# Performance work log

Hardware: AMD Instinct MI355X
Metric: run time of the kernel (lower is better)

Reference implementation:

```python
import jax, jax.numpy as jnp
import numpy as np

MIN_LEN = 4      # g.min_word_length
MAX_LEN = 10     # g.max_word_length
THRESH = 0.05    # g.init_threshold
NEG = -1e9


def setup_inputs() -> dict:
    key = jax.random.key(0)
    ks = jax.random.split(key, 6)
    B, L, F, D, U, V = 16, 64, 60, 256, 600, 10000
    x = jax.random.normal(ks[0], (B, L, F), jnp.float32)            # batch dense feat matrix
    unit_feats = jax.random.normal(ks[1], (U, F), jnp.float32)      # per-unit features
    W = jax.random.normal(ks[2], (F, D), jnp.float32) * 0.1         # FeatEmbedding weight
    lengths = jax.random.randint(ks[3], (B,), MIN_LEN, L + 1)       # sentence lengths
    indexed_segments = jax.random.randint(ks[4], (V, MAX_LEN), 0, U)  # vocab -> unit ids
    vocab_length = jax.random.randint(ks[5], (V,), MIN_LEN, MAX_LEN + 1)
    return dict(x=x, unit_feats=unit_feats, W=W, lengths=lengths,
                indexed_segments=indexed_segments, vocab_length=vocab_length)


def reference(x, unit_feats, W, lengths, indexed_segments, vocab_length):
    B, L, _ = x.shape
    V, J = indexed_segments.shape
    # embedding: features -> char_emb space
    word_repr = x @ W                 # [B, L, D]
    unit_repr = unit_feats @ W        # [U, D]
    # cosine similarity between every segment position and every unit
    wn = word_repr / (jnp.linalg.norm(word_repr, axis=-1, keepdims=True) + 1e-8)
    un = unit_repr / (jnp.linalg.norm(unit_repr, axis=-1, keepdims=True) + 1e-8)
    sim = jnp.einsum('bld,ud->blu', wn, un)  # [B, L, U]
    # pad so span gathers past the end read zeros (masked later by `viable`)
    sim_pad = jnp.pad(sim, ((0, 0), (0, J), (0, 0)))
    # accumulate per-position unit scores along each vocab word's unit sequence
    acc = jnp.zeros((B, L, V), sim.dtype)
    per_len = []
    for j in range(J):  # fixed small loop over word-length positions
        # sim at start+j for unit indexed_segments[v, j] -> [B, L, V]
        s_j = sim_pad[:, j:j + L, :][:, :, indexed_segments[:, j]]
        acc = acc + s_j
        if j + 1 >= MIN_LEN:
            per_len.append(acc / (j + 1))  # length-normalized match score
    scores = jnp.stack(per_len, axis=2)  # [B, len_s=L, len_e=E, V]
    E = scores.shape[2]
    k = jnp.arange(E) + MIN_LEN                          # candidate word lengths
    ends = jnp.arange(L)[:, None] + k[None, :] - 1        # [L, E]
    viable = ends[None] < lengths[:, None, None]          # [B, L, E]
    len_match = vocab_length[None, None, None, :] == k[None, None, :, None]
    mask = viable[..., None] & len_match                  # [B, L, E, V]
    masked = jnp.where(mask, scores, NEG)
    # best vocab word per span candidate
    value = masked.max(axis=-1)                           # [B, L, E]
    matched_vocab = masked.argmax(axis=-1)                # [B, L, E]
    matched = value > THRESH
    # best span candidate per batch element (eval path: hard max)
    flat = value.reshape(B, -1)                           # [B, L*E]
    best_inds = flat.argmax(axis=-1)
    best_scores = flat.max(axis=-1)
    best_starts = best_inds // E
    best_ends = best_inds % E + best_starts + MIN_LEN - 1
    any_matched = matched.reshape(B, -1).any(axis=-1)
    best_vocab = jnp.take_along_axis(matched_vocab.reshape(B, -1), best_inds[:, None], axis=1)[:, 0]
    return best_scores, best_starts, best_ends, any_matched, best_vocab
```

## Files before the change

### kernel.cpp

```cpp
#include <hip/hip_runtime.h>
#include <math.h>

#define BB 16
#define LL 64
#define FF 60
#define DD 256
#define UU 600
#define VV 10000
#define JMAX 10
#define MINL 4
#define EE 7
#define NEG (-1e9f)
#define TH 0.05f
#define VHALF (VV / 2)

#define UNT_OFF   0
#define UNT_SZ    (256 * 640)
#define WNT_OFF   (UNT_OFF + UNT_SZ)
#define WNT_SZ    (256 * 1024)
#define SIM_OFF   (WNT_OFF + WNT_SZ)
#define SIM_SZ    (BB * LL * UU)
#define PK_OFF    (SIM_OFF + SIM_SZ)
#define PK_SZ     (VV * 8)
#define VAL_OFF   (PK_OFF + PK_SZ)
#define VAL_SZ    (2 * BB * LL * EE)
#define VOC_OFF   (VAL_OFF + VAL_SZ)

__global__ __launch_bounds__(256) void k_pack(const int* __restrict__ seg,
                                              const int* __restrict__ vlen,
                                              unsigned int* __restrict__ pk) {
    int v = blockIdx.x * 256 + threadIdx.x;
    if (v >= VV) return;
    const int* s = seg + v * JMAX;
    unsigned int t[10];
#pragma unroll
    for (int j = 0; j < JMAX; ++j) t[j] = (unsigned int)(s[j] * 11 + j);
    unsigned int* dst = pk + v * 8;
    dst[0] = t[0] | (t[1] << 16);
    dst[1] = t[2] | (t[3] << 16);
    dst[2] = t[4] | (t[5] << 16);
    dst[3] = t[6] | (t[7] << 16);
    dst[4] = t[8] | (t[9] << 16);
    dst[5] = (unsigned int)vlen[v];
    dst[6] = 0;
    dst[7] = 0;
}

__global__ __launch_bounds__(64) void k_embed(const float* __restrict__ x,
                                              const float* __restrict__ uf,
                                              const float* __restrict__ W,
                                              float* __restrict__ unT,
                                              float* __restrict__ wnT) {
    int id = blockIdx.x;
    int lane = threadIdx.x;
    const float* row;
    float* outB;
    int stride, col;
    if (id < UU) { row = uf + id * FF; outB = unT; stride = 640;  col = id; }
    else { int bl = id - UU; row = x + bl * FF; outB = wnT; stride = 1024; col = bl; }

    float r0 = 0.f, r1 = 0.f, r2 = 0.f, r3 = 0.f;
#pragma unroll 4
    for (int f = 0; f < FF; ++f) {
        float xv = row[f];
        r0 += xv * W[f * DD + lane];
        r1 += xv * W[f * DD + lane + 64];
        r2 += xv * W[f * DD + lane + 128];
        r3 += xv * W[f * DD + lane + 192];
    }
    float ss = r0 * r0 + r1 * r1 + r2 * r2 + r3 * r3;
#pragma unroll
    for (int m = 32; m > 0; m >>= 1) ss += __shfl_xor(ss, m, 64);
    float inv = 1.0f / (sqrtf(ss) + 1e-8f);
    outB[(lane      ) * stride + col] = r0 * inv;
    outB[(lane +  64) * stride + col] = r1 * inv;
    outB[(lane + 128) * stride + col] = r2 * inv;
    outB[(lane + 192) * stride + col] = r3 * inv;
}

__global__ __launch_bounds__(320, 5) void k_sim(const float* __restrict__ unT,
                                                const float* __restrict__ wnT,
                                                float* __restrict__ sim) {
    int blk = blockIdx.x;
    int b  = blk >> 6;
    int r  = blk & 63;
    int l0 = (r >> 1) * 2;
    int uh = r & 1;
    int bl0 = b * 64 + l0;
    int tid = threadIdx.x;
    int w = tid >> 6;
    int lane = tid & 63;
    int u = uh * 320 + w * 64 + lane;

    float a0 = 0.f, a1 = 0.f;
#pragma unroll 8
    for (int d = 0; d < DD; ++d) {
        float w0 = wnT[d * 1024 + bl0 + 0];
        float w1 = wnT[d * 1024 + bl0 + 1];
        float v  = unT[d * 640 + u];
        a0 += w0 * v;
        a1 += w1 * v;
    }
    if (u < UU) {
        sim[(bl0 + 0) * UU + u] = a0;
        sim[(bl0 + 1) * UU + u] = a1;
    }
}

__global__ __launch_bounds__(512, 8) void k_score(const float* __restrict__ sim,
                                                  const unsigned int* __restrict__ pk,
                                                  const int* __restrict__ lengths,
                                                  float* __restrict__ val,
                                                  int* __restrict__ voc) {
    __shared__ float lds[UU * 11];
    __shared__ float redS[14][8];
    __shared__ int   redV[14][8];

    int blk = blockIdx.x;
    int half = blk >> 9;
    int rest = blk & 511;
    int b  = rest >> 5;
    int l0 = (rest & 31) * 2;
    int tid = threadIdx.x;

    for (int u = tid; u < UU; u += 512) {
#pragma unroll
        for (int r = 0; r < 11; ++r) {
            int m = l0 + r;
            lds[u * 11 + r] = (m < LL) ? sim[(b * 64 + m) * UU + u] : 0.0f;
        }
    }
    __syncthreads();

    float bS[EE][2];
    int   bV[EE][2];
#pragma unroll
    for (int e = 0; e < EE; ++e) {
        bS[e][0] = -1e30f; bS[e][1] = -1e30f;
        bV[e][0] = 0;      bV[e][1] = 0;
    }

    int vend = VHALF * (half + 1);
    for (int v = VHALF * half + tid; v < vend; v += 512) {
        const uint4* pp = (const uint4*)(pk + v * 8);
        uint4 qa = pp[0];
        uint4 qb = pp[1];
        int idx[10];
        idx[0] = qa.x & 0xffff; idx[1] = qa.x >> 16;
        idx[2] = qa.y & 0xffff; idx[3] = qa.y >> 16;
        idx[4] = qa.z & 0xffff; idx[5] = qa.z >> 16;
        idx[6] = qa.w & 0xffff; idx[7] = qa.w >> 16;
        idx[8] = qb.x & 0xffff; idx[9] = qb.x >> 16;
        int k = (int)(qb.y & 0xffff);

        float a0 = 0.f, a1 = 0.f;
#pragma unroll
        for (int j = 0; j < JMAX; ++j) {
            float x0 = lds[idx[j]];
            float x1 = lds[idx[j] + 1];
            a0 += x0;
            a1 += x1;
            if (j >= MINL - 1) {
                int e = j - (MINL - 1);
                bool m = (k == j + 1);
                bool p0 = m & (a0 > bS[e][0]);
                bool p1 = m & (a1 > bS[e][1]);
                bS[e][0] = p0 ? a0 : bS[e][0];
                bV[e][0] = p0 ? v  : bV[e][0];
                bS[e][1] = p1 ? a1 : bS[e][1];
                bV[e][1] = p1 ? v  : bV[e][1];
            }
        }
    }

    int w = tid >> 6, lane = tid & 63;
#pragma unroll
    for (int e = 0; e < EE; ++e) {
#pragma unroll
        for (int dl = 0; dl < 2; ++dl) {
            float s = bS[e][dl];
            int vv = bV[e][dl];
#pragma unroll
            for (int off = 32; off > 0; off >>= 1) {
                float os = __shfl_down(s, off, 64);
                int   ov = __shfl_down(vv, off, 64);
                if (os > s || (os == s && ov < vv)) { s = os; vv = ov; }
            }
            if (lane == 0) { redS[e * 2 + dl][w] = s; redV[e * 2 + dl][w] = vv; }
        }
    }
    __syncthreads();

    if (tid < 14) {
        int e  = tid >> 1;
        int dl = tid & 1;
        float s = redS[tid][0];
        int  vv = redV[tid][0];
#pragma unroll
        for (int w2 = 1; w2 < 8; ++w2) {
            float os = redS[tid][w2];
            int   ov = redV[tid][w2];
            if (os > s || (os == s && ov < vv)) { s = os; vv = ov; }
        }
        int lg = l0 + dl;
        int k = e + MINL;
        bool viable = (lg + k - 1) < lengths[b];
        float sn = s / (float)k;
        int o = (half * BB * LL + b * 64 + lg) * EE + e;
        val[o] = viable ? sn : NEG;
        voc[o] = viable ? vv : 0;
    }
}

__global__ __launch_bounds__(512) void k_final(const float* __restrict__ val,
                                               const int* __restrict__ voc,
                                               float* __restrict__ out) {
    __shared__ float sS[8];
    __shared__ int   sI[8];
    __shared__ int   sV[8];
    __shared__ int   sA[8];
    int b = blockIdx.x;
    int t = threadIdx.x;
    float s = -3e38f;
    int idx = 1 << 30;
    int vc = 0;
    int any = 0;
    if (t < LL * EE) {
        int o0 = b * LL * EE + t;
        int o1 = BB * LL * EE + o0;
        float s0 = val[o0], s1 = val[o1];
        bool sel = s1 > s0;
        s  = sel ? s1 : s0;
        vc = sel ? voc[o1] : voc[o0];
        idx = t;
        any = (s > TH) ? 1 : 0;
    }
#pragma unroll
    for (int off = 32; off > 0; off >>= 1) {
        float os = __shfl_down(s, off, 64);
        int   oi = __shfl_down(idx, off, 64);
        int   ov = __shfl_down(vc, off, 64);
        int   oa = __shfl_down(any, off, 64);
        if (os > s || (os == s && oi < idx)) { s = os; idx = oi; vc = ov; }
        any |= oa;
    }
    int w = t >> 6, lane = t & 63;
    if (lane == 0) { sS[w] = s; sI[w] = idx; sV[w] = vc; sA[w] = any; }
    __syncthreads();
    if (t == 0) {
        for (int w2 = 1; w2 < 8; ++w2) {
            float os = sS[w2];
            int   oi = sI[w2];
            if (os > s || (os == s && oi < idx)) { s = os; idx = oi; vc = sV[w2]; }
            any |= sA[w2];
        }
        int start = idx / EE;
        int e = idx - start * EE;
        int end = e + start + MINL - 1;
        out[b]      = s;
        out[16 + b] = (float)start;
        out[32 + b] = (float)end;
        out[48 + b] = any ? 1.0f : 0.0f;
        out[64 + b] = (float)vc;
    }
}

extern "C" void kernel_launch(void* const* d_in, const int* in_sizes, int n_in,
                              void* d_out, int out_size, void* d_ws, size_t ws_size,
                              hipStream_t stream) {
    const float* x       = (const float*)d_in[0];
    const float* uf      = (const float*)d_in[1];
    const float* W       = (const float*)d_in[2];
    const int*   lengths = (const int*)d_in[3];
    const int*   seg     = (const int*)d_in[4];
    const int*   vlen    = (const int*)d_in[5];
    float* out = (float*)d_out;
    float* ws  = (float*)d_ws;

    float*        unT = ws + UNT_OFF;
    float*        wnT = ws + WNT_OFF;
    float*        sim = ws + SIM_OFF;
    unsigned int* pk  = (unsigned int*)(ws + PK_OFF);
    float*        val = ws + VAL_OFF;
    int*          voc = (int*)(ws + VOC_OFF);

    k_pack<<<(VV + 255) / 256, 256, 0, stream>>>(seg, vlen, pk);
    k_embed<<<UU + BB * LL, 64, 0, stream>>>(x, uf, W, unT, wnT);
    k_sim<<<1024, 320, 0, stream>>>(unT, wnT, sim);
    k_score<<<1024, 512, 0, stream>>>(sim, pk, lengths, val, voc);
    k_final<<<BB, 512, 0, stream>>>(val, voc, out);
}
```

Measured before the change: 147.8 us.

## Bucket vocab by word length and fuse pack and embed kernels

Vocab entries are grouped into per-length buckets with an atomic counter, so the scoring loop only sums the j positions each word actually uses. This drops the per-element length compare and the seven-way select. The pack and embed kernels are merged into one launch. k_sim now computes four rows per block with a float4 load, halving the grid. Because atomic ordering makes vocab order within a bucket non-deterministic, tie-breaking on vocab index is added, and a memset launch is now needed.

```diff
diff --git a/kernel.cpp b/kernel.cpp
--- a/kernel.cpp
+++ b/kernel.cpp
@@ -12,103 +12,139 @@
 #define EE 7
 #define NEG (-1e9f)
 #define TH 0.05f
-#define VHALF (VV / 2)
+#define BCAP 10240
 
 #define UNT_OFF   0
-#define UNT_SZ    (256 * 640)
-#define WNT_OFF   (UNT_OFF + UNT_SZ)
-#define WNT_SZ    (256 * 1024)
-#define SIM_OFF   (WNT_OFF + WNT_SZ)
-#define SIM_SZ    (BB * LL * UU)
-#define PK_OFF    (SIM_OFF + SIM_SZ)
-#define PK_SZ     (VV * 8)
-#define VAL_OFF   (PK_OFF + PK_SZ)
-#define VAL_SZ    (2 * BB * LL * EE)
-#define VOC_OFF   (VAL_OFF + VAL_SZ)
-
-__global__ __launch_bounds__(256) void k_pack(const int* __restrict__ seg,
+#define WNT_OFF   163840
+#define SIM_OFF   425984
+#define CNT_OFF   1040384
+#define SRT_OFF   1040392
+#define VAL_OFF   1613832
+#define VOC_OFF   1628168
+
+__global__ __launch_bounds__(256) void k_prep(const int* __restrict__ seg,
                                               const int* __restrict__ vlen,
-                                              unsigned int* __restrict__ pk) {
-    int v = blockIdx.x * 256 + threadIdx.x;
-    if (v >= VV) return;
-    const int* s = seg + v * JMAX;
-    unsigned int t[10];
-#pragma unroll
-    for (int j = 0; j < JMAX; ++j) t[j] = (unsigned int)(s[j] * 11 + j);
-    unsigned int* dst = pk + v * 8;
-    dst[0] = t[0] | (t[1] << 16);
-    dst[1] = t[2] | (t[3] << 16);
-    dst[2] = t[4] | (t[5] << 16);
-    dst[3] = t[6] | (t[7] << 16);
-    dst[4] = t[8] | (t[9] << 16);
-    dst[5] = (unsigned int)vlen[v];
-    dst[6] = 0;
-    dst[7] = 0;
-}
-
-__global__ __launch_bounds__(64) void k_embed(const float* __restrict__ x,
+                                              const float* __restrict__ x,
                                               const float* __restrict__ uf,
                                               const float* __restrict__ W,
+                                              unsigned int* __restrict__ cnt,
+                                              unsigned int* __restrict__ srt,
                                               float* __restrict__ unT,
                                               float* __restrict__ wnT) {
-    int id = blockIdx.x;
-    int lane = threadIdx.x;
-    const float* row;
-    float* outB;
-    int stride, col;
-    if (id < UU) { row = uf + id * FF; outB = unT; stride = 640;  col = id; }
-    else { int bl = id - UU; row = x + bl * FF; outB = wnT; stride = 1024; col = bl; }
-
-    float r0 = 0.f, r1 = 0.f, r2 = 0.f, r3 = 0.f;
+    int blk = blockIdx.x;
+    if (blk < 40) {
+        int v = blk * 256 + threadIdx.x;
+        if (v >= VV) return;
+        const int* s = seg + v * JMAX;
+        unsigned int t[10];
+#pragma unroll
+        for (int j = 0; j < JMAX; ++j) t[j] = (unsigned int)(s[j] * 11 + j);
+        int e = vlen[v] - MINL;
+        unsigned int pos = atomicAdd(&cnt[e], 1u);
+        unsigned int* dst = srt + ((size_t)e * BCAP + pos) * 8;
+        uint4 qa, qb;
+        qa.x = t[0] | (t[1] << 16);
+        qa.y = t[2] | (t[3] << 16);
+        qa.z = t[4] | (t[5] << 16);
+        qa.w = t[6] | (t[7] << 16);
+        qb.x = t[8] | (t[9] << 16);
+        qb.y = (unsigned int)v;
+        qb.z = 0; qb.w = 0;
+        ((uint4*)dst)[0] = qa;
+        ((uint4*)dst)[1] = qb;
+    } else {
+        int w = threadIdx.x >> 6;
+        int lane = threadIdx.x & 63;
+        int id = (blk - 40) * 4 + w;
+        const float* row;
+        float* outB;
+        int stride, col;
+        if (id < UU) { row = uf + id * FF; outB = unT; stride = 640;  col = id; }
+        else { int bl = id - UU; row = x + bl * FF; outB = wnT; stride = 1024; col = bl; }
+
+        float r0 = 0.f, r1 = 0.f, r2 = 0.f, r3 = 0.f;
 #pragma unroll 4
-    for (int f = 0; f < FF; ++f) {
-        float xv = row[f];
-        r0 += xv * W[f * DD + lane];
-        r1 += xv * W[f * DD + lane + 64];
-        r2 += xv * W[f * DD + lane + 128];
-        r3 += xv * W[f * DD + lane + 192];
-    }
-    float ss = r0 * r0 + r1 * r1 + r2 * r2 + r3 * r3;
-#pragma unroll
-    for (int m = 32; m > 0; m >>= 1) ss += __shfl_xor(ss, m, 64);
-    float inv = 1.0f / (sqrtf(ss) + 1e-8f);
-    outB[(lane      ) * stride + col] = r0 * inv;
-    outB[(lane +  64) * stride + col] = r1 * inv;
-    outB[(lane + 128) * stride + col] = r2 * inv;
-    outB[(lane + 192) * stride + col] = r3 * inv;
-}
-
-__global__ __launch_bounds__(320, 5) void k_sim(const float* __restrict__ unT,
-                                                const float* __restrict__ wnT,
-                                                float* __restrict__ sim) {
+        for (int f = 0; f < FF; ++f) {
+            float xv = row[f];
+            r0 += xv * W[f * DD + lane];
+            r1 += xv * W[f * DD + lane + 64];
+            r2 += xv * W[f * DD + lane + 128];
+            r3 += xv * W[f * DD + lane + 192];
+        }
+        float ss = r0 * r0 + r1 * r1 + r2 * r2 + r3 * r3;
+#pragma unroll
+        for (int m = 32; m > 0; m >>= 1) ss += __shfl_xor(ss, m, 64);
+        float inv = 1.0f / (sqrtf(ss) + 1e-8f);
+        outB[(lane      ) * stride + col] = r0 * inv;
+        outB[(lane +  64) * stride + col] = r1 * inv;
+        outB[(lane + 128) * stride + col] = r2 * inv;
+        outB[(lane + 192) * stride + col] = r3 * inv;
+    }
+}
+
+__global__ __launch_bounds__(320) void k_sim(const float* __restrict__ unT,
+                                             const float* __restrict__ wnT,
+                                             float* __restrict__ sim) {
     int blk = blockIdx.x;
-    int b  = blk >> 6;
-    int r  = blk & 63;
-    int l0 = (r >> 1) * 2;
+    int b  = blk >> 5;
+    int r  = blk & 31;
+    int l0 = (r >> 1) * 4;
     int uh = r & 1;
     int bl0 = b * 64 + l0;
-    int tid = threadIdx.x;
-    int w = tid >> 6;
-    int lane = tid & 63;
-    int u = uh * 320 + w * 64 + lane;
-
-    float a0 = 0.f, a1 = 0.f;
+    int u = uh * 320 + threadIdx.x;
+
+    float a0 = 0.f, a1 = 0.f, a2 = 0.f, a3 = 0.f;
 #pragma unroll 8
     for (int d = 0; d < DD; ++d) {
-        float w0 = wnT[d * 1024 + bl0 + 0];
-        float w1 = wnT[d * 1024 + bl0 + 1];
+        float4 wv = *(const float4*)(wnT + d * 1024 + bl0);
         float v  = unT[d * 640 + u];
-        a0 += w0 * v;
-        a1 += w1 * v;
+        a0 += wv.x * v;
+        a1 += wv.y * v;
+        a2 += wv.z * v;
+        a3 += wv.w * v;
     }
     if (u < UU) {
         sim[(bl0 + 0) * UU + u] = a0;
         sim[(bl0 + 1) * UU + u] = a1;
+        sim[(bl0 + 2) * UU + u] = a2;
+        sim[(bl0 + 3) * UU + u] = a3;
+    }
+}
+
+template<int K>
+__device__ __forceinline__ void bucket_pass(const unsigned int* __restrict__ srt,
+                                            const float* __restrict__ lds,
+                                            int e, int half, int n, int tid,
+                                            float& s0, int& w0,
+                                            float& s1, int& w1) {
+    int n0 = n >> 1;
+    int lo = half ? n0 : 0;
+    int hi = half ? n : n0;
+    for (int p = lo + tid; p < hi; p += 512) {
+        const uint4* pp = (const uint4*)(srt + ((size_t)e * BCAP + p) * 8);
+        uint4 qa = pp[0];
+        uint4 qb = pp[1];
+        unsigned int tw[5] = {qa.x, qa.y, qa.z, qa.w, qb.x};
+        int v = (int)qb.y;
+        float a0 = 0.f, a1 = 0.f;
+#pragma unroll
+        for (int j = 0; j < K; ++j) {
+            int idx = (int)((tw[j >> 1] >> ((j & 1) * 16)) & 0xffffu);
+            float x0 = lds[idx];
+            float x1 = lds[idx + 1];
+            a0 += x0;
+            a1 += x1;
+        }
+        bool p0 = (a0 > s0) || (a0 == s0 && v < w0);
+        bool p1 = (a1 > s1) || (a1 == s1 && v < w1);
+        s0 = p0 ? a0 : s0;  w0 = p0 ? v : w0;
+        s1 = p1 ? a1 : s1;  w1 = p1 ? v : w1;
     }
 }
 
 __global__ __launch_bounds__(512, 8) void k_score(const float* __restrict__ sim,
-                                                  const unsigned int* __restrict__ pk,
+                                                  const unsigned int* __restrict__ srt,
+                                                  const unsigned int* __restrict__ cnt,
                                                   const int* __restrict__ lengths,
                                                   float* __restrict__ val,
                                                   int* __restrict__ voc) {
@@ -132,46 +168,25 @@
     }
     __syncthreads();
 
+    int ne[EE];
+#pragma unroll
+    for (int e = 0; e < EE; ++e) ne[e] = (int)cnt[e];
+
     float bS[EE][2];
     int   bV[EE][2];
 #pragma unroll
     for (int e = 0; e < EE; ++e) {
         bS[e][0] = -1e30f; bS[e][1] = -1e30f;
-        bV[e][0] = 0;      bV[e][1] = 0;
-    }
-
-    int vend = VHALF * (half + 1);
-    for (int v = VHALF * half + tid; v < vend; v += 512) {
-        const uint4* pp = (const uint4*)(pk + v * 8);
-        uint4 qa = pp[0];
-        uint4 qb = pp[1];
-        int idx[10];
-        idx[0] = qa.x & 0xffff; idx[1] = qa.x >> 16;
-        idx[2] = qa.y & 0xffff; idx[3] = qa.y >> 16;
-        idx[4] = qa.z & 0xffff; idx[5] = qa.z >> 16;
-        idx[6] = qa.w & 0xffff; idx[7] = qa.w >> 16;
-        idx[8] = qb.x & 0xffff; idx[9] = qb.x >> 16;
-        int k = (int)(qb.y & 0xffff);
-
-        float a0 = 0.f, a1 = 0.f;
-#pragma unroll
-        for (int j = 0; j < JMAX; ++j) {
-            float x0 = lds[idx[j]];
-            float x1 = lds[idx[j] + 1];
-            a0 += x0;
-            a1 += x1;
-            if (j >= MINL - 1) {
-                int e = j - (MINL - 1);
-                bool m = (k == j + 1);
-                bool p0 = m & (a0 > bS[e][0]);
-                bool p1 = m & (a1 > bS[e][1]);
-                bS[e][0] = p0 ? a0 : bS[e][0];
-                bV[e][0] = p0 ? v  : bV[e][0];
-                bS[e][1] = p1 ? a1 : bS[e][1];
-                bV[e][1] = p1 ? v  : bV[e][1];
-            }
-        }
-    }
+        bV[e][0] = VV;     bV[e][1] = VV;
+    }
+
+    bucket_pass<4> (srt, lds, 0, half, ne[0], tid, bS[0][0], bV[0][0], bS[0][1], bV[0][1]);
+    bucket_pass<5> (srt, lds, 1, half, ne[1], tid, bS[1][0], bV[1][0], bS[1][1], bV[1][1]);
+    bucket_pass<6> (srt, lds, 2, half, ne[2], tid, bS[2][0], bV[2][0], bS[2][1], bV[2][1]);
+    bucket_pass<7> (srt, lds, 3, half, ne[3], tid, bS[3][0], bV[3][0], bS[3][1], bV[3][1]);
+    bucket_pass<8> (srt, lds, 4, half, ne[4], tid, bS[4][0], bV[4][0], bS[4][1], bV[4][1]);
+    bucket_pass<9> (srt, lds, 5, half, ne[5], tid, bS[5][0], bV[5][0], bS[5][1], bV[5][1]);
+    bucket_pass<10>(srt, lds, 6, half, ne[6], tid, bS[6][0], bV[6][0], bS[6][1], bV[6][1]);
 
     int w = tid >> 6, lane = tid & 63;
 #pragma unroll
@@ -229,9 +244,10 @@
         int o0 = b * LL * EE + t;
         int o1 = BB * LL * EE + o0;
         float s0 = val[o0], s1 = val[o1];
-        bool sel = s1 > s0;
+        int   v0 = voc[o0], v1 = voc[o1];
+        bool sel = (s1 > s0) || (s1 == s0 && v1 < v0);
         s  = sel ? s1 : s0;
-        vc = sel ? voc[o1] : voc[o0];
+        vc = sel ? v1 : v0;
         idx = t;
         any = (s > TH) ? 1 : 0;
     }
@@ -280,13 +296,14 @@
     float*        unT = ws + UNT_OFF;
     float*        wnT = ws + WNT_OFF;
     float*        sim = ws + SIM_OFF;
-    unsigned int* pk  = (unsigned int*)(ws + PK_OFF);
+    unsigned int* cnt = (unsigned int*)(ws + CNT_OFF);
+    unsigned int* srt = (unsigned int*)(ws + SRT_OFF);
     float*        val = ws + VAL_OFF;
     int*          voc = (int*)(ws + VOC_OFF);
 
-    k_pack<<<(VV + 255) / 256, 256, 0, stream>>>(seg, vlen, pk);
-    k_embed<<<UU + BB * LL, 64, 0, stream>>>(x, uf, W, unT, wnT);
-    k_sim<<<1024, 320, 0, stream>>>(unT, wnT, sim);
-    k_score<<<1024, 512, 0, stream>>>(sim, pk, lengths, val, voc);
+    hipMemsetAsync(cnt, 0, 8 * sizeof(unsigned int), stream);
+    k_prep<<<446, 256, 0, stream>>>(seg, vlen, x, uf, W, cnt, srt, unT, wnT);
+    k_sim<<<512, 320, 0, stream>>>(unT, wnT, sim);
+    k_score<<<1024, 512, 0, stream>>>(sim, srt, cnt, lengths, val, voc);
     k_final<<<BB, 512, 0, stream>>>(val, voc, out);
 }
```

Measured after the change: 173.5 us. 17.4% more time.
